# Performance work log

Hardware: AMD Instinct MI355X
Metric: run time of the kernel (lower is better)

Reference implementation:

```python
import jax, jax.numpy as jnp
import numpy as np

H, D = 8, 8          # num_heads, hidden_size (head dim)
SCALE = 0.25         # Hopfield beta/scaling
STEPS = 3            # update_steps_max
LN_EPS = 1e-5


def ln(x, g, b):
    m = x.mean(-1, keepdims=True)
    v = ((x - m) ** 2).mean(-1, keepdims=True)
    return (x - m) * jax.lax.rsqrt(v + LN_EPS) * g + b


def setup_inputs() -> dict:
    key = jax.random.key(0)
    ks = jax.random.split(key, 8)
    B, N, E = 32, 512, 512
    P = H * D  # 64 virtual hopfield dim
    s = lambda k, shape: jax.random.normal(k, shape, jnp.float32) * 0.05
    return dict(
        x=jax.random.normal(ks[0], (B, N, E), jnp.float32),
        g_q=jnp.ones((E,), jnp.float32), b_q=jnp.zeros((E,), jnp.float32),
        g_k=jnp.ones((E,), jnp.float32), b_k=jnp.zeros((E,), jnp.float32),
        g_v=jnp.ones((E,), jnp.float32), b_v=jnp.zeros((E,), jnp.float32),
        Wq=s(ks[1], (P, E)), bq=jnp.zeros((P,), jnp.float32),
        Wk=s(ks[2], (P, E)), bk=jnp.zeros((P,), jnp.float32),
        Wv=s(ks[3], (P, E)), bv=jnp.zeros((P,), jnp.float32),
        Wo=s(ks[4], (E, P)), bo=jnp.zeros((E,), jnp.float32),
        Wl=s(ks[5], (1, N * E)), bl=jnp.zeros((1,), jnp.float32),
    )


def reference(x, g_q, b_q, g_k, b_k, g_v, b_v,
              Wq, bq, Wk, bk, Wv, bv, Wo, bo, Wl, bl):
    B, N, E = x.shape
    # LayerNorm on state (query), stored (key), projection (value) patterns
    q = (ln(x, g_q, b_q) @ Wq.T + bq).reshape(B, N, H, D)
    k = (ln(x, g_k, b_k) @ Wk.T + bk).reshape(B, N, H, D)
    v = (ln(x, g_v, b_v) @ Wv.T + bv).reshape(B, N, H, D)
    # iterative Hopfield retrieval: xi <- softmax(beta * xi K^T) K
    xi = q
    for _ in range(STEPS):
        a = jax.nn.softmax(SCALE * jnp.einsum('bihd,bjhd->bhij', xi, k), axis=-1)
        xi = jnp.einsum('bhij,bjhd->bihd', a, k)
    # final association with value patterns
    a = jax.nn.softmax(SCALE * jnp.einsum('bihd,bjhd->bhij', xi, k), axis=-1)
    o = jnp.einsum('bhij,bjhd->bihd', a, v).reshape(B, N, H * D)
    o = o @ Wo.T + bo              # (B, N, E) out projection
    y = o.reshape(B, N * E) @ Wl.T + bl  # (B, 1) classifier head
    return y.reshape(-1)           # flatten(start_dim=0) -> (B,)
```

## Files before the change

### kernel.cpp

```cpp
#include <hip/hip_runtime.h>

#define E_DIM 512
#define N_DIM 512
#define B_DIM 32
#define H_DIM 8
#define D_DIM 8
#define P3    192

typedef _Float16 half_t;
typedef __attribute__((ext_vector_type(2))) _Float16 half2v;
typedef __attribute__((ext_vector_type(4))) _Float16 half4v;
typedef __attribute__((ext_vector_type(8))) _Float16 half8v;
typedef __attribute__((ext_vector_type(4))) float f32x4;

#define XS_STRIDE 520
#define KB2_STRIDE 20
#define KT_STRIDE  532

__device__ inline float block_reduce_256(float v) {
    __shared__ float red[4];
    #pragma unroll
    for (int m = 32; m >= 1; m >>= 1) v += __shfl_xor(v, m);
    int w = threadIdx.x >> 6;
    if ((threadIdx.x & 63) == 0) red[w] = v;
    __syncthreads();
    if (threadIdx.x == 0) v = red[0] + red[1] + red[2] + red[3];
    return v;
}

__device__ inline half8v cvt8(float4 a, float4 b) {
    half8v h;
    h[0] = (half_t)a.x; h[1] = (half_t)a.y; h[2] = (half_t)a.z; h[3] = (half_t)a.w;
    h[4] = (half_t)b.x; h[5] = (half_t)b.y; h[6] = (half_t)b.z; h[7] = (half_t)b.w;
    return h;
}

__device__ inline half2v pk2(float a, float b) {
    return __builtin_bit_cast(half2v, __builtin_amdgcn_cvt_pkrtz(a, b));
}

__global__ __launch_bounds__(256) void prep_w(const float* __restrict__ Wq,
                        const float* __restrict__ Wk, const float* __restrict__ Wv,
                        const float* __restrict__ gq, const float* __restrict__ gk,
                        const float* __restrict__ gv,
                        const float* __restrict__ bnq, const float* __restrict__ bnk,
                        const float* __restrict__ bnv,
                        const float* __restrict__ bq, const float* __restrict__ bk,
                        const float* __restrict__ bv,
                        const float* __restrict__ bl,
                        half_t* __restrict__ WthF, float* __restrict__ colsum,
                        float* __restrict__ b2, float* __restrict__ y,
                        float* __restrict__ c0acc) {
    int pp = blockIdx.x;
    int which = pp >> 6, p = pp & 63;
    int ct = pp >> 4, c16 = pp & 15;
    const float* W  = (which == 0) ? Wq  : (which == 1) ? Wk  : Wv;
    const float* g  = (which == 0) ? gq  : (which == 1) ? gk  : gv;
    const float* bn = (which == 0) ? bnq : (which == 1) ? bnk : bnv;
    const float* bb = (which == 0) ? bq  : (which == 1) ? bk  : bv;
    int t = threadIdx.x;
    if (pp == 0) {
        if (t < 32) y[t] = bl[0];
        if (t == 32) c0acc[0] = 0.f;
    }
    float cs = 0.f, dt = 0.f;
    #pragma unroll
    for (int l = 0; l < 2; ++l) {
        int e = t + l * 256;
        float wv = W[p * E_DIM + e];
        half_t wh = (half_t)(wv * g[e]);
        int k32 = e >> 5, g2 = (e >> 3) & 3, j = e & 7;
        WthF[(((size_t)(ct * 16 + k32) * 64) + g2 * 16 + c16) * 8 + j] = wh;
        cs += (float)wh;
        dt += wv * bn[e];
    }
    cs = block_reduce_256(cs);
    __syncthreads();
    dt = block_reduce_256(dt);
    if (t == 0) { colsum[pp] = cs; b2[pp] = dt + bb[p]; }
}

__global__ __launch_bounds__(256) void ln_qkv_wl2(const float* __restrict__ x,
                                              const half_t* __restrict__ WthF,
                                              const float* __restrict__ b2,
                                              const float* __restrict__ colsum,
                                              half_t* __restrict__ qkv16,
                                              const float* __restrict__ Wl,
                                              const float* __restrict__ Wo,
                                              const float* __restrict__ bo,
                                              float* __restrict__ Wl2,
                                              float* __restrict__ c0acc) {
    __shared__ half_t Xs[16 * XS_STRIDE];
    __shared__ float stats[16][2];
    if (blockIdx.x < 1024) {
        const int t = threadIdx.x;
        const int lane = t & 63;
        const int w = t >> 6;
        const int g2 = lane >> 4, c16 = lane & 15;
        const int row0 = blockIdx.x * 16;
        {
            const int row = t >> 4, c = t & 15;
            const float4* xrow = (const float4*)(x + (size_t)(row0 + row) * E_DIM);
            float sx = 0.f, sxx = 0.f;
            #pragma unroll
            for (int l = 0; l < 8; ++l) {
                int f4 = c + l * 16;
                float4 a = xrow[f4];
                sx  += a.x + a.y + a.z + a.w;
                sxx += a.x*a.x + a.y*a.y + a.z*a.z + a.w*a.w;
                half4v h;
                h[0] = (half_t)a.x; h[1] = (half_t)a.y;
                h[2] = (half_t)a.z; h[3] = (half_t)a.w;
                *(half4v*)&Xs[row * XS_STRIDE + f4 * 4] = h;
            }
            #pragma unroll
            for (int m = 1; m <= 8; m <<= 1) {
                sx += __shfl_xor(sx, m); sxx += __shfl_xor(sxx, m);
            }
            if (c == 0) {
                float mean = sx * (1.f / E_DIM);
                float var  = sxx * (1.f / E_DIM) - mean * mean;
                stats[row][0] = mean;
                stats[row][1] = rsqrtf(var + 1e-5f);
            }
        }
        __syncthreads();
        f32x4 acc[3] = {{0.f,0.f,0.f,0.f},{0.f,0.f,0.f,0.f},{0.f,0.f,0.f,0.f}};
        const half_t* wf = WthF + (size_t)w * 3 * 16 * 512;
        #pragma unroll 4
        for (int k32 = 0; k32 < 16; ++k32) {
            half8v af = *(const half8v*)&Xs[c16 * XS_STRIDE + k32 * 32 + g2 * 8];
            #pragma unroll
            for (int nt = 0; nt < 3; ++nt) {
                half8v bf = *(const half8v*)(wf + ((size_t)(nt * 16 + k32)) * 512 + lane * 8);
                acc[nt] = __builtin_amdgcn_mfma_f32_16x16x32_f16(af, bf, acc[nt], 0, 0, 0);
            }
        }
        #pragma unroll
        for (int nt = 0; nt < 3; ++nt) {
            int pp = w * 48 + nt * 16 + c16;
            float cs = colsum[pp], bb = b2[pp];
            int which = pp >> 6, p = pp & 63;
            int h = p >> 3, d = p & 7;
            half_t* dst0 = qkv16 + (size_t)which * (B_DIM * H_DIM * N_DIM * D_DIM);
            #pragma unroll
            for (int r = 0; r < 4; ++r) {
                int rowi = g2 * 4 + r;
                float val = stats[rowi][1] * (acc[nt][r] - stats[rowi][0] * cs) + bb;
                int ng = row0 + rowi;
                int b = ng >> 9, n = ng & 511;
                dst0[(((size_t)(b * H_DIM + h)) * N_DIM + n) * D_DIM + d] = (half_t)val;
            }
        }
    } else {
        const int blk = blockIdx.x - 1024;
        const int t = threadIdx.x;
        const int lane = t & 63;
        const int w = t >> 6;
        const int g2 = lane >> 4, c16 = lane & 15;
        const int n0 = blk * 16;
        const int pcol = w * 16;
        f32x4 acc = {0.f, 0.f, 0.f, 0.f};
        float pc = 0.f;
        const float* arow = Wl + (size_t)(n0 + c16) * E_DIM;
        #pragma unroll 2
        for (int k0 = 0; k0 < E_DIM; k0 += 32) {
            int kbase = k0 + g2 * 8;
            float4 a0 = *(const float4*)(arow + kbase);
            float4 a1 = *(const float4*)(arow + kbase + 4);
            if (w == 0) {
                float4 b0 = *(const float4*)(bo + kbase);
                float4 b1 = *(const float4*)(bo + kbase + 4);
                pc += a0.x*b0.x + a0.y*b0.y + a0.z*b0.z + a0.w*b0.w
                    + a1.x*b1.x + a1.y*b1.y + a1.z*b1.z + a1.w*b1.w;
            }
            half8v af = cvt8(a0, a1);
            half8v bf;
            #pragma unroll
            for (int j = 0; j < 8; ++j)
                bf[j] = (half_t)Wo[(size_t)(kbase + j) * 64 + pcol + c16];
            acc = __builtin_amdgcn_mfma_f32_16x16x32_f16(af, bf, acc, 0, 0, 0);
        }
        int p = pcol + c16, h = p >> 3, d = p & 7;
        #pragma unroll
        for (int r = 0; r < 4; ++r) {
            int n = n0 + g2 * 4 + r;
            Wl2[h * (N_DIM * D_DIM) + n * D_DIM + d] = acc[r];
        }
        if (w == 0) {
            pc += __shfl_xor(pc, 16); pc += __shfl_xor(pc, 32);
            pc += __shfl_xor(pc, 1);  pc += __shfl_xor(pc, 2);
            pc += __shfl_xor(pc, 4);  pc += __shfl_xor(pc, 8);
            if (lane == 0) atomicAdd(c0acc, pc);
        }
    }
}

__global__ __launch_bounds__(256) void hopfield(const half_t* __restrict__ q16,
                                                const half_t* __restrict__ k16,
                                                const half_t* __restrict__ v16,
                                                const float* __restrict__ Wl2,
                                                const float* __restrict__ c0acc,
                                                float* __restrict__ y) {
    __shared__ half_t Kb2[N_DIM * KB2_STRIDE];
    __shared__ half_t KTb[16 * KT_STRIDE];
    __shared__ half_t Xi[128 * 8 + 16];
    const int t = threadIdx.x;
    const int lane = t & 63;
    const int w = t >> 6;
    const int g2 = lane >> 4;
    const int c16 = lane & 15;
    const int bh = blockIdx.x >> 2, seg = blockIdx.x & 3;
    const float C = 0.25f * 1.44269504088896f;
    const half_t* kg = k16 + (size_t)bh * (N_DIM * D_DIM);
    const half_t* vg = v16 + (size_t)bh * (N_DIM * D_DIM);
    const half_t* qg = q16 + (size_t)bh * (N_DIM * D_DIM) + seg * 128 * 8;
    const float* wl2p = Wl2 + (bh & 7) * (N_DIM * D_DIM) + seg * 128 * 8;

    {
        const int j0 = 2 * t;
        half8v r0 = *(const half8v*)(kg + j0 * 8);
        half8v r1 = *(const half8v*)(kg + j0 * 8 + 8);
        const half4v z4 = {};
        half_t* p0 = &Kb2[j0 * KB2_STRIDE];
        half_t* p1 = &Kb2[(j0 + 1) * KB2_STRIDE];
        *(half4v*)(p0)      = __builtin_shufflevector(r0, r0, 0, 1, 2, 3);
        *(half4v*)(p0 + 4)  = __builtin_shufflevector(r0, r0, 4, 5, 6, 7);
        *(half4v*)(p0 + 8)  = z4;
        *(half4v*)(p0 + 12) = z4;
        *(half4v*)(p0 + 16) = z4;
        *(half4v*)(p1)      = __builtin_shufflevector(r1, r1, 0, 1, 2, 3);
        *(half4v*)(p1 + 4)  = __builtin_shufflevector(r1, r1, 4, 5, 6, 7);
        *(half4v*)(p1 + 8)  = z4;
        *(half4v*)(p1 + 12) = z4;
        *(half4v*)(p1 + 16) = z4;
        #pragma unroll
        for (int d = 0; d < 8; ++d) {
            KTb[d * KT_STRIDE + j0]     = r0[d];
            KTb[d * KT_STRIDE + j0 + 1] = r1[d];
        }
        KTb[8 * KT_STRIDE + j0]     = (half_t)1.f;
        KTb[8 * KT_STRIDE + j0 + 1] = (half_t)1.f;
    }
    if (t < 128) {
        half8v hq = *(const half8v*)(qg + t * 8);
        half8v h;
        #pragma unroll
        for (int d = 0; d < 8; ++d) h[d] = (half_t)(C * (float)hq[d]);
        *(half8v*)&Xi[t * 8] = h;
    }
    __syncthreads();

    const half_t* akp = &Kb2[c16 * KB2_STRIDE + g2 * 4];
    const half_t* aTp = &KTb[c16 * KT_STRIDE + g2 * 4];
    const half4v hz = {};
    float fsum = 0.f;

    for (int it = 0; it < 4; ++it) {
        if (it == 3) {
            __syncthreads();
            const int j0 = 2 * t;
            half8v r0 = *(const half8v*)(vg + j0 * 8);
            half8v r1 = *(const half8v*)(vg + j0 * 8 + 8);
            #pragma unroll
            for (int d = 0; d < 8; ++d) {
                KTb[d * KT_STRIDE + j0]     = r0[d];
                KTb[d * KT_STRIDE + j0 + 1] = r1[d];
            }
            __syncthreads();
        }
        half4v bx0 = *(const half4v*)&Xi[(w * 32 + c16) * 8 + g2 * 4];
        half4v bx1 = *(const half4v*)&Xi[(w * 32 + 16 + c16) * 8 + g2 * 4];
        if (g2 >= 2) { bx0 = hz; bx1 = hz; }
        f32x4 U0 = {0.f, 0.f, 0.f, 0.f}, U1 = {0.f, 0.f, 0.f, 0.f};
        #pragma unroll 4
        for (int kt = 0; kt < 32; ++kt) {
            half4v ak = *(const half4v*)(akp + kt * (16 * KB2_STRIDE));
            half4v aT = *(const half4v*)(aTp + kt * 16);
            f32x4 Z = {0.f, 0.f, 0.f, 0.f};
            f32x4 S0 = __builtin_amdgcn_mfma_f32_16x16x16f16(ak, bx0, Z, 0, 0, 0);
            f32x4 S1 = __builtin_amdgcn_mfma_f32_16x16x16f16(ak, bx1, Z, 0, 0, 0);
            half2v l0 = pk2(__builtin_amdgcn_exp2f(S0[0]), __builtin_amdgcn_exp2f(S0[1]));
            half2v h0 = pk2(__builtin_amdgcn_exp2f(S0[2]), __builtin_amdgcn_exp2f(S0[3]));
            half4v p0 = __builtin_shufflevector(l0, h0, 0, 1, 2, 3);
            half2v l1 = pk2(__builtin_amdgcn_exp2f(S1[0]), __builtin_amdgcn_exp2f(S1[1]));
            half2v h1 = pk2(__builtin_amdgcn_exp2f(S1[2]), __builtin_amdgcn_exp2f(S1[3]));
            half4v p1 = __builtin_shufflevector(l1, h1, 0, 1, 2, 3);
            U0 = __builtin_amdgcn_mfma_f32_16x16x16f16(aT, p0, U0, 0, 0, 0);
            U1 = __builtin_amdgcn_mfma_f32_16x16x16f16(aT, p1, U1, 0, 0, 0);
        }
        float den0 = __shfl(U0[0], 32 + c16, 64);
        float den1 = __shfl(U1[0], 32 + c16, 64);
        float inv0 = __builtin_amdgcn_rcpf(den0);
        float inv1 = __builtin_amdgcn_rcpf(den1);
        if (it < 3) {
            if (g2 < 2) {
                half4v h0, h1;
                #pragma unroll
                for (int r = 0; r < 4; ++r) {
                    h0[r] = (half_t)(U0[r] * (C * inv0));
                    h1[r] = (half_t)(U1[r] * (C * inv1));
                }
                *(half4v*)&Xi[(w * 32 + c16) * 8 + g2 * 4]      = h0;
                *(half4v*)&Xi[(w * 32 + 16 + c16) * 8 + g2 * 4] = h1;
            }
        } else {
            if (g2 < 2) {
                float4 w0 = *(const float4*)&wl2p[(w * 32 + c16) * 8 + g2 * 4];
                float4 w1 = *(const float4*)&wl2p[(w * 32 + 16 + c16) * 8 + g2 * 4];
                fsum = inv0 * (U0[0]*w0.x + U0[1]*w0.y + U0[2]*w0.z + U0[3]*w0.w)
                     + inv1 * (U1[0]*w1.x + U1[1]*w1.y + U1[2]*w1.z + U1[3]*w1.w);
            }
        }
    }
    float tot = block_reduce_256(fsum);
    if (t == 0) atomicAdd(&y[bh >> 3], tot);
    if (blockIdx.x == 0 && t < 32) {
        atomicAdd(&y[t], c0acc[0]);
    }
}

extern "C" void kernel_launch(void* const* d_in, const int* in_sizes, int n_in,
                              void* d_out, int out_size, void* d_ws, size_t ws_size,
                              hipStream_t stream) {
    const float* x   = (const float*)d_in[0];
    const float* g_q = (const float*)d_in[1];
    const float* b_q = (const float*)d_in[2];
    const float* g_k = (const float*)d_in[3];
    const float* b_k = (const float*)d_in[4];
    const float* g_v = (const float*)d_in[5];
    const float* b_v = (const float*)d_in[6];
    const float* Wq  = (const float*)d_in[7];
    const float* bq  = (const float*)d_in[8];
    const float* Wk  = (const float*)d_in[9];
    const float* bk  = (const float*)d_in[10];
    const float* Wv  = (const float*)d_in[11];
    const float* bv  = (const float*)d_in[12];
    const float* Wo  = (const float*)d_in[13];
    const float* bo  = (const float*)d_in[14];
    const float* Wl  = (const float*)d_in[15];
    const float* bl  = (const float*)d_in[16];
    float* out = (float*)d_out;

    float* ws = (float*)d_ws;
    float*  colsum = ws;
    float*  b2     = ws + 192;
    float*  c0acc  = ws + 384;
    float*  Wl2    = ws + 448;
    half_t* WthF   = (half_t*)(ws + 33216);
    half_t* qkv16  = (half_t*)(ws + 82368);

    half_t* q16 = qkv16;
    half_t* k16 = qkv16 + 1048576;
    half_t* v16 = qkv16 + 2097152;

    prep_w    <<<192, 256, 0, stream>>>(Wq, Wk, Wv, g_q, g_k, g_v,
                                        b_q, b_k, b_v, bq, bk, bv, bl,
                                        WthF, colsum, b2, out, c0acc);
    ln_qkv_wl2<<<1056, 256, 0, stream>>>(x, WthF, b2, colsum, qkv16,
                                         Wl, Wo, bo, Wl2, c0acc);
    hopfield  <<<1024, 256, 0, stream>>>(q16, k16, v16, Wl2, c0acc, out);
}
```

Before: 157.9 us.

## Split Hopfield queries into eight segments with compact shared memory layout

The hopfield kernel now splits each batch-head's 512 queries into 8 blocks of 64 instead of 4 blocks of 128, so each wave handles one 16-query tile rather than two. Launch bounds ask for 8 blocks per SM. Shared memory is packed into one buffer: the padded Kb2 array is replaced by a dense K copy plus a zero strip that lanes with g2>=2 read, and the K-transpose stores are vectorized to half2. The goal is more blocks in flight, better latency hiding and less LDS per block. The cost is that every block reloads K and V from global memory twice as often, and each wave has less independent MFMA work to overlap.

```diff
diff --git a/kernel.cpp b/kernel.cpp
--- a/kernel.cpp
+++ b/kernel.cpp
@@ -14,8 +14,13 @@
 typedef __attribute__((ext_vector_type(4))) float f32x4;
 
 #define XS_STRIDE 520
-#define KB2_STRIDE 20
-#define KT_STRIDE  532
+
+#define SM_KT0 0
+#define SM_KB0 4800
+#define SM_Z0  8896
+#define SM_XI0 9408
+#define SM_TOT 9936
+#define KT_STRIDE 532
 
 __device__ inline float block_reduce_256(float v) {
     __shared__ float red[4];
@@ -196,63 +201,60 @@
     }
 }
 
-__global__ __launch_bounds__(256) void hopfield(const half_t* __restrict__ q16,
-                                                const half_t* __restrict__ k16,
-                                                const half_t* __restrict__ v16,
-                                                const float* __restrict__ Wl2,
-                                                const float* __restrict__ c0acc,
-                                                float* __restrict__ y) {
-    __shared__ half_t Kb2[N_DIM * KB2_STRIDE];
-    __shared__ half_t KTb[16 * KT_STRIDE];
-    __shared__ half_t Xi[128 * 8 + 16];
+__global__ __launch_bounds__(256, 8) void hopfield(const half_t* __restrict__ q16,
+                                                   const half_t* __restrict__ k16,
+                                                   const half_t* __restrict__ v16,
+                                                   const float* __restrict__ Wl2,
+                                                   const float* __restrict__ c0acc,
+                                                   float* __restrict__ y) {
+    __shared__ __align__(16) half_t sm[SM_TOT];
     const int t = threadIdx.x;
     const int lane = t & 63;
     const int w = t >> 6;
     const int g2 = lane >> 4;
     const int c16 = lane & 15;
-    const int bh = blockIdx.x >> 2, seg = blockIdx.x & 3;
+    const int bh = blockIdx.x >> 3, seg = blockIdx.x & 7;
     const float C = 0.25f * 1.44269504088896f;
     const half_t* kg = k16 + (size_t)bh * (N_DIM * D_DIM);
     const half_t* vg = v16 + (size_t)bh * (N_DIM * D_DIM);
-    const half_t* qg = q16 + (size_t)bh * (N_DIM * D_DIM) + seg * 128 * 8;
-    const float* wl2p = Wl2 + (bh & 7) * (N_DIM * D_DIM) + seg * 128 * 8;
+    const half_t* qg = q16 + (size_t)bh * (N_DIM * D_DIM) + seg * 64 * 8;
+    const float* wl2p = Wl2 + (bh & 7) * (N_DIM * D_DIM) + seg * 64 * 8;
 
     {
         const int j0 = 2 * t;
         half8v r0 = *(const half8v*)(kg + j0 * 8);
         half8v r1 = *(const half8v*)(kg + j0 * 8 + 8);
-        const half4v z4 = {};
-        half_t* p0 = &Kb2[j0 * KB2_STRIDE];
-        half_t* p1 = &Kb2[(j0 + 1) * KB2_STRIDE];
-        *(half4v*)(p0)      = __builtin_shufflevector(r0, r0, 0, 1, 2, 3);
-        *(half4v*)(p0 + 4)  = __builtin_shufflevector(r0, r0, 4, 5, 6, 7);
-        *(half4v*)(p0 + 8)  = z4;
-        *(half4v*)(p0 + 12) = z4;
-        *(half4v*)(p0 + 16) = z4;
-        *(half4v*)(p1)      = __builtin_shufflevector(r1, r1, 0, 1, 2, 3);
-        *(half4v*)(p1 + 4)  = __builtin_shufflevector(r1, r1, 4, 5, 6, 7);
-        *(half4v*)(p1 + 8)  = z4;
-        *(half4v*)(p1 + 12) = z4;
-        *(half4v*)(p1 + 16) = z4;
+        *(half8v*)&sm[SM_KB0 + j0 * 8]     = r0;
+        *(half8v*)&sm[SM_KB0 + j0 * 8 + 8] = r1;
         #pragma unroll
         for (int d = 0; d < 8; ++d) {
-            KTb[d * KT_STRIDE + j0]     = r0[d];
-            KTb[d * KT_STRIDE + j0 + 1] = r1[d];
-        }
-        KTb[8 * KT_STRIDE + j0]     = (half_t)1.f;
-        KTb[8 * KT_STRIDE + j0 + 1] = (half_t)1.f;
-    }
-    if (t < 128) {
-        half8v hq = *(const half8v*)(qg + t * 8);
-        half8v h;
-        #pragma unroll
-        for (int d = 0; d < 8; ++d) h[d] = (half_t)(C * (float)hq[d]);
-        *(half8v*)&Xi[t * 8] = h;
+            half2v p; p[0] = r0[d]; p[1] = r1[d];
+            *(half2v*)&sm[SM_KT0 + d * KT_STRIDE + j0] = p;
+        }
+        half2v one2; one2[0] = (half_t)1.f; one2[1] = (half_t)1.f;
+        *(half2v*)&sm[SM_KT0 + 8 * KT_STRIDE + j0] = one2;
+        if (t < 128) {
+            const half4v z4 = {};
+            *(half4v*)&sm[SM_Z0 + t * 4] = z4;
+        }
+        if (t < 6) {
+            half2v z2 = {};
+            *(half2v*)&sm[9 * KT_STRIDE + t * 2] = z2;
+        }
+        if (t < 64) {
+            half8v hq = *(const half8v*)(qg + t * 8);
+            half8v h;
+            #pragma unroll
+            for (int d = 0; d < 8; ++d) h[d] = (half_t)(C * (float)hq[d]);
+            *(half8v*)&sm[SM_XI0 + t * 8] = h;
+        }
     }
     __syncthreads();
 
-    const half_t* akp = &Kb2[c16 * KB2_STRIDE + g2 * 4];
-    const half_t* aTp = &KTb[c16 * KT_STRIDE + g2 * 4];
+    const half_t* aTp  = sm + SM_KT0 + c16 * KT_STRIDE + g2 * 4;
+    const half_t* akp0 = sm + ((g2 < 2) ? (SM_KB0 + c16 * 8 + g2 * 4) : SM_Z0);
+    const int akstep4  = (g2 < 2) ? 512 : 0;
+    const f32x4 Zf = {0.f, 0.f, 0.f, 0.f};
     const half4v hz = {};
     float fsum = 0.f;
 
@@ -264,52 +266,43 @@
             half8v r1 = *(const half8v*)(vg + j0 * 8 + 8);
             #pragma unroll
             for (int d = 0; d < 8; ++d) {
-                KTb[d * KT_STRIDE + j0]     = r0[d];
-                KTb[d * KT_STRIDE + j0 + 1] = r1[d];
+                half2v p; p[0] = r0[d]; p[1] = r1[d];
+                *(half2v*)&sm[SM_KT0 + d * KT_STRIDE + j0] = p;
             }
             __syncthreads();
         }
-        half4v bx0 = *(const half4v*)&Xi[(w * 32 + c16) * 8 + g2 * 4];
-        half4v bx1 = *(const half4v*)&Xi[(w * 32 + 16 + c16) * 8 + g2 * 4];
-        if (g2 >= 2) { bx0 = hz; bx1 = hz; }
-        f32x4 U0 = {0.f, 0.f, 0.f, 0.f}, U1 = {0.f, 0.f, 0.f, 0.f};
-        #pragma unroll 4
-        for (int kt = 0; kt < 32; ++kt) {
-            half4v ak = *(const half4v*)(akp + kt * (16 * KB2_STRIDE));
-            half4v aT = *(const half4v*)(aTp + kt * 16);
-            f32x4 Z = {0.f, 0.f, 0.f, 0.f};
-            f32x4 S0 = __builtin_amdgcn_mfma_f32_16x16x16f16(ak, bx0, Z, 0, 0, 0);
-            f32x4 S1 = __builtin_amdgcn_mfma_f32_16x16x16f16(ak, bx1, Z, 0, 0, 0);
-            half2v l0 = pk2(__builtin_amdgcn_exp2f(S0[0]), __builtin_amdgcn_exp2f(S0[1]));
-            half2v h0 = pk2(__builtin_amdgcn_exp2f(S0[2]), __builtin_amdgcn_exp2f(S0[3]));
-            half4v p0 = __builtin_shufflevector(l0, h0, 0, 1, 2, 3);
-            half2v l1 = pk2(__builtin_amdgcn_exp2f(S1[0]), __builtin_amdgcn_exp2f(S1[1]));
-            half2v h1 = pk2(__builtin_amdgcn_exp2f(S1[2]), __builtin_amdgcn_exp2f(S1[3]));
-            half4v p1 = __builtin_shufflevector(l1, h1, 0, 1, 2, 3);
-            U0 = __builtin_amdgcn_mfma_f32_16x16x16f16(aT, p0, U0, 0, 0, 0);
-            U1 = __builtin_amdgcn_mfma_f32_16x16x16f16(aT, p1, U1, 0, 0, 0);
-        }
-        float den0 = __shfl(U0[0], 32 + c16, 64);
-        float den1 = __shfl(U1[0], 32 + c16, 64);
-        float inv0 = __builtin_amdgcn_rcpf(den0);
-        float inv1 = __builtin_amdgcn_rcpf(den1);
+        half4v bx = *(const half4v*)&sm[SM_XI0 + (w * 16 + c16) * 8 + g2 * 4];
+        if (g2 >= 2) bx = hz;
+        f32x4 U = Zf;
+        const half_t* ap = akp0;
+        #pragma unroll 2
+        for (int k4 = 0; k4 < 8; ++k4) {
+            #pragma unroll
+            for (int u = 0; u < 4; ++u) {
+                const int kt = k4 * 4 + u;
+                half4v ak = *(const half4v*)(ap + u * 128);
+                half4v aT = *(const half4v*)(aTp + kt * 16);
+                f32x4 S = __builtin_amdgcn_mfma_f32_16x16x16f16(ak, bx, Zf, 0, 0, 0);
+                half2v lo = pk2(__builtin_amdgcn_exp2f(S[0]), __builtin_amdgcn_exp2f(S[1]));
+                half2v hi = pk2(__builtin_amdgcn_exp2f(S[2]), __builtin_amdgcn_exp2f(S[3]));
+                half4v p = __builtin_shufflevector(lo, hi, 0, 1, 2, 3);
+                U = __builtin_amdgcn_mfma_f32_16x16x16f16(aT, p, U, 0, 0, 0);
+            }
+            ap += akstep4;
+        }
+        float den = __shfl(U[0], 32 + c16, 64);
+        float inv = __builtin_amdgcn_rcpf(den);
         if (it < 3) {
             if (g2 < 2) {
-                half4v h0, h1;
+                half4v h;
                 #pragma unroll
-                for (int r = 0; r < 4; ++r) {
-                    h0[r] = (half_t)(U0[r] * (C * inv0));
-                    h1[r] = (half_t)(U1[r] * (C * inv1));
-                }
-                *(half4v*)&Xi[(w * 32 + c16) * 8 + g2 * 4]      = h0;
-                *(half4v*)&Xi[(w * 32 + 16 + c16) * 8 + g2 * 4] = h1;
+                for (int r = 0; r < 4; ++r) h[r] = (half_t)(U[r] * (C * inv));
+                *(half4v*)&sm[SM_XI0 + (w * 16 + c16) * 8 + g2 * 4] = h;
             }
         } else {
             if (g2 < 2) {
-                float4 w0 = *(const float4*)&wl2p[(w * 32 + c16) * 8 + g2 * 4];
-                float4 w1 = *(const float4*)&wl2p[(w * 32 + 16 + c16) * 8 + g2 * 4];
-                fsum = inv0 * (U0[0]*w0.x + U0[1]*w0.y + U0[2]*w0.z + U0[3]*w0.w)
-                     + inv1 * (U1[0]*w1.x + U1[1]*w1.y + U1[2]*w1.z + U1[3]*w1.w);
+                float4 w0 = *(const float4*)&wl2p[(w * 16 + c16) * 8 + g2 * 4];
+                fsum = inv * (U[0]*w0.x + U[1]*w0.y + U[2]*w0.z + U[3]*w0.w);
             }
         }
     }
@@ -359,5 +352,5 @@
                                         WthF, colsum, b2, out, c0acc);
     ln_qkv_wl2<<<1056, 256, 0, stream>>>(x, WthF, b2, colsum, qkv16,
                                          Wl, Wo, bo, Wl2, c0acc);
-    hopfield  <<<1024, 256, 0, stream>>>(q16, k16, v16, Wl2, c0acc, out);
-}
+    hopfield  <<<2048, 256, 0, stream>>>(q16, k16, v16, Wl2, c0acc, out);
+}
```

Result: no change. 159.7 us (+1.1%).
